# Kernel tuning notes

Measured on AMD Instinct MI355X. Metric: run time of the kernel, lower is better.

The kernel has to match this reference:

```python
import jax, jax.numpy as jnp
import numpy as np

EPS = 1e-8

def l2norm(x, axis):
    # matches torch: x / (sqrt(sum(x^2)) + eps)
    return x / (jnp.sqrt(jnp.sum(x * x, axis=axis, keepdims=True)) + EPS)

def setup_inputs() -> dict:
    key = jax.random.key(0)
    kq, kc, kwq, kbq, kwk, kbk = jax.random.split(key, 6)
    B, QL, SL, D = 128, 512, 1024, 1024
    query = jax.random.normal(kq, (B, QL, D), dtype=jnp.float32)
    context = jax.random.normal(kc, (B, SL, D), dtype=jnp.float32)
    s = 1.0 / np.sqrt(D)
    Wq = jax.random.uniform(kwq, (D, D), jnp.float32, -s, s)
    bq = jax.random.uniform(kbq, (D,), jnp.float32, -s, s)
    Wk = jax.random.uniform(kwk, (D, D), jnp.float32, -s, s)
    bk = jax.random.uniform(kbk, (D,), jnp.float32, -s, s)
    return {"query": query, "context": context, "Wq": Wq, "bq": bq,
            "Wk": Wk, "bk": bk, "smooth": 9.0}

def reference(query, context, Wq, bq, Wk, bk, smooth):
    # linear projections (nn.Linear: x @ W^T + b)
    sim_k = jnp.einsum('bsd,ed->bse', context, Wk) + bk   # (B, SL, D)
    sim_q = jnp.einsum('bqd,ed->bqe', query, Wq) + bq     # (B, QL, D)
    # scores: bmm(sim_k, sim_q^T) -> (B, SL, QL)
    attn = jnp.einsum('bse,bqe->bsq', sim_k, sim_q)
    attn = jnp.where(attn >= 0, attn, 0.1 * attn)          # LeakyReLU(0.1)
    attn = l2norm(attn, axis=2)                            # over queryL dim
    # transpose -> (B, QL, SL), scale, softmax over sourceL
    attn = jax.nn.softmax(attn.transpose(0, 2, 1) * smooth, axis=2)
    # weighted sum of raw context (sim_v = context; fcv unused in original)
    wc = jnp.einsum('bqs,bsd->bqd', attn, context)         # (B, QL, D)
    return l2norm(wc, axis=-1)
```

## Files before the change

kernel.cpp:

```cpp
#include <hip/hip_runtime.h>
#include <hip/hip_bf16.h>

typedef __attribute__((ext_vector_type(8))) short bf16x8;
typedef __attribute__((ext_vector_type(4))) float f32x4;
typedef __attribute__((ext_vector_type(4))) unsigned short u16x4;
typedef __attribute__((ext_vector_type(8))) unsigned short u16x8;

#define DEVINL static __device__ __forceinline__

DEVINL unsigned short f2bf(float f) {
  union { float f; unsigned u; } a; a.f = f;
  return (unsigned short)((a.u + 0x7fffu + ((a.u >> 16) & 1u)) >> 16);
}
DEVINL float bf2f(unsigned short s) {
  union { unsigned u; float f; } a; a.u = ((unsigned)s) << 16; return a.f;
}

typedef __attribute__((address_space(1))) const unsigned char ga_u8;
typedef __attribute__((address_space(3))) unsigned char ls_u8;

constexpr int KD = 1024;
constexpr int NKT = KD / 64;


#define STAGE(b_, mat_, kt_) do { \
    const unsigned short* src_ = (mat_) == 0 ? Az : Bz; \
    const int br_ = (mat_) == 0 ? m0 : n0; \
    char* dst_ = lds + (b_) * 65536 + (mat_) * 32768; \
    _Pragma("unroll") \
    for (int i_ = 0; i_ < 4; ++i_) { \
      const unsigned short* g_ = src_ + (size_t)(br_ + i_ * 64 + sr) * KD + (kt_) * 64 + gc * 8; \
      __builtin_amdgcn_global_load_lds((ga_u8*)g_, (ls_u8*)(dst_ + (i_ * 512 + wv * 64) * 16), 16, 0, 0); \
    } \
  } while (0)

#define STAGE2(b_, kt_) do { STAGE(b_, 0, kt_); STAGE(b_, 1, kt_); } while (0)

#define KSUB(b_, ks_, STG) do { \
    const char* pA_ = lds + (b_) * 65536; \
    const char* pB_ = pA_ + 32768; \
    const int co_ = (((ks_) * 4 + kg) ^ (ml & 7)) << 4; \
    bf16x8 af_[8], bf_[4]; \
    _Pragma("unroll") \
    for (int mi = 0; mi < 8; ++mi) \
      af_[mi] = *(const bf16x8*)(pA_ + (wm * 128 + mi * 16 + ml) * 128 + co_); \
    _Pragma("unroll") \
    for (int ni = 0; ni < 4; ++ni) \
      bf_[ni] = *(const bf16x8*)(pB_ + (wn * 64 + ni * 16 + ml) * 128 + co_); \
    STG; \
    __builtin_amdgcn_s_setprio(1); \
    _Pragma("unroll") \
    for (int mi = 0; mi < 8; ++mi) \
    _Pragma("unroll") \
    for (int ni = 0; ni < 4; ++ni) \
      acc[mi][ni] = __builtin_amdgcn_mfma_f32_16x16x32_bf16(af_[mi], bf_[ni], acc[mi][ni], 0, 0, 0); \
    __builtin_amdgcn_s_setprio(0); \
  } while (0)

template<int MODE>
__global__ __launch_bounds__(512, 2) void gemm8(
    const unsigned short* __restrict__ A, const unsigned short* __restrict__ B,
    const float* __restrict__ bias, void* __restrict__ Cv,
    float* __restrict__ rnorm2, int mtiles,
    long long sAz, long long sBz, long long sCz, long long sRz, long long sBiasz)
{
  alignas(16) __shared__ char lds[131072];

  const int tid = threadIdx.x;
  const int lane = tid & 63;
  const int wv = tid >> 6;
  const int wm = wv >> 2;
  const int wn = wv & 3;
  const int kg = lane >> 4;
  const int ml = lane & 15;

  const int nwg = (int)gridDim.x;
  const int bid = (int)blockIdx.x;
  const int w = (bid & 7) * (nwg >> 3) + (bid >> 3);
  const int bpz = mtiles * 4;
  const int z = w / bpz;
  const int rem = w - z * bpz;
  const int mt = rem >> 2, nt = rem & 3;
  const int m0 = mt * 256, n0 = nt * 256;

  const unsigned short* Az = A + (size_t)z * (size_t)sAz;
  const unsigned short* Bz = B + (size_t)z * (size_t)sBz;

  const int sr = tid >> 3;
  const int gc = (tid & 7) ^ (sr & 7);

  f32x4 acc[8][4];
  const f32x4 zero4 = {0.f, 0.f, 0.f, 0.f};
#pragma unroll
  for (int i = 0; i < 8; ++i)
#pragma unroll
    for (int j = 0; j < 4; ++j) acc[i][j] = zero4;

  STAGE2(0, 0);
  asm volatile("s_waitcnt vmcnt(0)" ::: "memory");
  __builtin_amdgcn_s_barrier();

  for (int t = 0; t < NKT; ++t) {
    const int cur = t & 1;
    const int nxt = cur ^ 1;
    if (t + 1 < NKT) {
      KSUB(cur, 0, STAGE2(nxt, t + 1));
      KSUB(cur, 1, );
    } else {
      KSUB(cur, 0, );
      KSUB(cur, 1, );
    }
    asm volatile("s_waitcnt vmcnt(0)" ::: "memory");
    __builtin_amdgcn_s_barrier();
  }

  float* ew = (float*)(lds + wv * 4352);
  const int erow = lane >> 3;
  const int ec8 = (lane & 7) * 8;
  const int ncol0 = n0 + wn * 64;

  if (MODE == 1 || MODE == 5) {
    const float* cb = bias + (size_t)z * (size_t)sBiasz;
    f32x4 cb4[8];
#pragma unroll
    for (int mi = 0; mi < 8; ++mi)
      cb4[mi] = *(const f32x4*)(cb + m0 + wm * 128 + mi * 16 + kg * 4);
    float* rn = rnorm2 + (size_t)z * (size_t)sRz;
#pragma unroll
    for (int ni = 0; ni < 4; ++ni) {
      float cs = 0.f;
#pragma unroll
      for (int mi = 0; mi < 8; ++mi)
#pragma unroll
        for (int j = 0; j < 4; ++j) {
          float v = acc[mi][ni][j] + cb4[mi][j];
          v = v >= 0.f ? v : 0.1f * v;
          acc[mi][ni][j] = v;
          cs += v * v;
        }
      cs += __shfl_xor(cs, 16);
      cs += __shfl_xor(cs, 32);
      if (kg == 0) atomicAdd(&rn[ncol0 + ni * 16 + ml], cs);
    }
  }

  f32x4 bv0 = zero4, bv1 = zero4;
  if (MODE == 0) {
    bv0 = *(const f32x4*)(bias + ncol0 + ec8);
    bv1 = *(const f32x4*)(bias + ncol0 + ec8 + 4);
  }

  float* rsq = (MODE == 4) ? rnorm2 + (size_t)z * (size_t)sRz : nullptr;

#pragma unroll
  for (int mi = 0; mi < 8; ++mi) {
#pragma unroll
    for (int ni = 0; ni < 4; ++ni)
#pragma unroll
      for (int j = 0; j < 4; ++j)
        ew[(kg * 4 + j) * 68 + ni * 16 + ml] = acc[mi][ni][j];
    const int rb = m0 + wm * 128 + mi * 16;
#pragma unroll
    for (int i = 0; i < 2; ++i) {
      const int r = erow + 8 * i;
      f32x4 x = *(const f32x4*)(&ew[r * 68 + ec8]);
      f32x4 y = *(const f32x4*)(&ew[r * 68 + ec8 + 4]);
      if (MODE == 4) {
        float ss = x[0]*x[0] + x[1]*x[1] + x[2]*x[2] + x[3]*x[3] +
                   y[0]*y[0] + y[1]*y[1] + y[2]*y[2] + y[3]*y[3];
        ss += __shfl_xor(ss, 1);
        ss += __shfl_xor(ss, 2);
        ss += __shfl_xor(ss, 4);
        if ((lane & 7) == 0) atomicAdd(&rsq[rb + r], ss);
      }
      if (MODE == 0 || MODE == 3 || MODE == 4 || MODE == 5) {
        unsigned short* C = (unsigned short*)Cv + (size_t)z * (size_t)sCz;
        union { unsigned short s[8]; u16x8 v; } u;
        u.s[0]=f2bf(x[0]+bv0[0]); u.s[1]=f2bf(x[1]+bv0[1]);
        u.s[2]=f2bf(x[2]+bv0[2]); u.s[3]=f2bf(x[3]+bv0[3]);
        u.s[4]=f2bf(y[0]+bv1[0]); u.s[5]=f2bf(y[1]+bv1[1]);
        u.s[6]=f2bf(y[2]+bv1[2]); u.s[7]=f2bf(y[3]+bv1[3]);
        *(u16x8*)(C + (size_t)(rb + r) * 1024 + ncol0 + ec8) = u.v;
      } else {
        float* C = (float*)Cv + (size_t)z * (size_t)sCz;
        *(f32x4*)(C + (size_t)(rb + r) * 1024 + ncol0 + ec8) = x;
        *(f32x4*)(C + (size_t)(rb + r) * 1024 + ncol0 + ec8 + 4) = y;
      }
    }
  }
}

__global__ __launch_bounds__(256) void wT_k(
    const float* __restrict__ W, unsigned short* __restrict__ WT)
{
  __shared__ float tile[32][36];
  const int t = threadIdx.x;
  const int e0 = blockIdx.x * 32, d0 = blockIdx.y * 32;
  const int r = t >> 3, c4 = (t & 7) * 4;
  f32x4 v = *(const f32x4*)(W + (size_t)(e0 + r) * 1024 + d0 + c4);
  *(f32x4*)(&tile[r][c4]) = v;
  __syncthreads();
  u16x4 o;
  o[0] = f2bf(tile[c4 + 0][r]); o[1] = f2bf(tile[c4 + 1][r]);
  o[2] = f2bf(tile[c4 + 2][r]); o[3] = f2bf(tile[c4 + 3][r]);
  *(u16x4*)(WT + (size_t)(d0 + r) * 1024 + e0 + c4) = o;
}

__global__ __launch_bounds__(256) void convert_ctx_k(
    const float* __restrict__ src, unsigned short* __restrict__ dstT,
    unsigned short* __restrict__ dstR)
{
  __shared__ float tile[32][36];
  const int t = threadIdx.x;
  const int s0 = blockIdx.x * 32, d0 = blockIdx.y * 32;
  const float* S = src + (size_t)blockIdx.z * 1048576;
  unsigned short* DT = dstT + (size_t)blockIdx.z * 1048576;
  unsigned short* DR = dstR + (size_t)blockIdx.z * 1048576;
  const int s = t >> 3, d4 = (t & 7) * 4;
  f32x4 v = *(const f32x4*)(S + (size_t)(s0 + s) * 1024 + d0 + d4);
  u16x4 r;
  r[0] = f2bf(v[0]); r[1] = f2bf(v[1]); r[2] = f2bf(v[2]); r[3] = f2bf(v[3]);
  *(u16x4*)(DR + (size_t)(s0 + s) * 1024 + d0 + d4) = r;
  *(f32x4*)(&tile[s][d4]) = v;
  __syncthreads();
  const int d = t >> 3, s4 = (t & 7) * 4;
  u16x4 o;
  o[0] = f2bf(tile[s4 + 0][d]); o[1] = f2bf(tile[s4 + 1][d]);
  o[2] = f2bf(tile[s4 + 2][d]); o[3] = f2bf(tile[s4 + 3][d]);
  *(u16x4*)(DT + (size_t)(d0 + d) * 1024 + s0 + s4) = o;
}

__global__ __launch_bounds__(256) void rowdot_k(
    const unsigned short* __restrict__ Mbf, const float* __restrict__ vec,
    float* __restrict__ outv)
{
  __shared__ float shs[4];
  const int t = threadIdx.x;
  const unsigned short* row = Mbf + (size_t)blockIdx.x * 1024;
  u16x4 a = *(const u16x4*)(row + t * 4);
  f32x4 b = *(const f32x4*)(vec + t * 4);
  float d = bf2f(a[0]) * b[0] + bf2f(a[1]) * b[1] +
            bf2f(a[2]) * b[2] + bf2f(a[3]) * b[3];
#pragma unroll
  for (int o = 32; o; o >>= 1) d += __shfl_xor(d, o);
  if ((t & 63) == 0) shs[t >> 6] = d;
  __syncthreads();
  if (t == 0) outv[blockIdx.x] = shs[0] + shs[1] + shs[2] + shs[3];
}

__global__ __launch_bounds__(256) void dot1_k(
    const float* __restrict__ a, const float* __restrict__ b,
    float* __restrict__ outv)
{
  __shared__ float shs[4];
  const int t = threadIdx.x;
  f32x4 x = ((const f32x4*)a)[t];
  f32x4 y = ((const f32x4*)b)[t];
  float d = x[0]*y[0] + x[1]*y[1] + x[2]*y[2] + x[3]*y[3];
#pragma unroll
  for (int o = 32; o; o >>= 1) d += __shfl_xor(d, o);
  if ((t & 63) == 0) shs[t >> 6] = d;
  __syncthreads();
  if (t == 0) outv[0] = shs[0] + shs[1] + shs[2] + shs[3];
}

__global__ __launch_bounds__(128) void cvtq_dot_k(
    const float* __restrict__ q, const float* __restrict__ vb,
    const float* __restrict__ bqbk, unsigned short* __restrict__ qbf,
    float* __restrict__ cq)
{
  __shared__ float sh[2];
  const int t = threadIdx.x;
  const size_t base = (size_t)blockIdx.x * 1024 + t * 8;
  f32x4 x = *(const f32x4*)(q + base);
  f32x4 y = *(const f32x4*)(q + base + 4);
  f32x4 v0 = *(const f32x4*)(vb + t * 8);
  f32x4 v1 = *(const f32x4*)(vb + t * 8 + 4);
  union { unsigned short s[8]; u16x8 v; } u;
  u.s[0]=f2bf(x[0]); u.s[1]=f2bf(x[1]); u.s[2]=f2bf(x[2]); u.s[3]=f2bf(x[3]);
  u.s[4]=f2bf(y[0]); u.s[5]=f2bf(y[1]); u.s[6]=f2bf(y[2]); u.s[7]=f2bf(y[3]);
  *(u16x8*)(qbf + base) = u.v;
  float d = x[0]*v0[0] + x[1]*v0[1] + x[2]*v0[2] + x[3]*v0[3] +
            y[0]*v1[0] + y[1]*v1[1] + y[2]*v1[2] + y[3]*v1[3];
#pragma unroll
  for (int o = 32; o; o >>= 1) d += __shfl_xor(d, o);
  if ((t & 63) == 0) sh[t >> 6] = d;
  __syncthreads();
  if (t == 0) cq[blockIdx.x] = sh[0] + sh[1] + bqbk[0];
}

__global__ __launch_bounds__(256) void softmax_k(
    const unsigned short* __restrict__ S, const float* __restrict__ rnorm2,
    const float* __restrict__ smoothp, unsigned short* __restrict__ P)
{
  __shared__ float shm[4], shs[4];
  const int t = threadIdx.x;
  const int z = blockIdx.x >> 9;
  const float sm = *smoothp;
  u16x4 sr = ((const u16x4*)(S + (size_t)blockIdx.x * 1024))[t];
  f32x4 r4 = ((const f32x4*)(rnorm2 + (size_t)z * 1024))[t];
  f32x4 lg;
  lg[0] = sm * bf2f(sr[0]) / (sqrtf(r4[0]) + 1e-8f);
  lg[1] = sm * bf2f(sr[1]) / (sqrtf(r4[1]) + 1e-8f);
  lg[2] = sm * bf2f(sr[2]) / (sqrtf(r4[2]) + 1e-8f);
  lg[3] = sm * bf2f(sr[3]) / (sqrtf(r4[3]) + 1e-8f);
  float mx = fmaxf(fmaxf(lg[0], lg[1]), fmaxf(lg[2], lg[3]));
#pragma unroll
  for (int o = 32; o; o >>= 1) mx = fmaxf(mx, __shfl_xor(mx, o));
  if ((t & 63) == 0) shm[t >> 6] = mx;
  __syncthreads();
  mx = fmaxf(fmaxf(shm[0], shm[1]), fmaxf(shm[2], shm[3]));
  f32x4 e;
  e[0] = __expf(lg[0] - mx); e[1] = __expf(lg[1] - mx);
  e[2] = __expf(lg[2] - mx); e[3] = __expf(lg[3] - mx);
  float sum = e[0] + e[1] + e[2] + e[3];
#pragma unroll
  for (int o = 32; o; o >>= 1) sum += __shfl_xor(sum, o);
  if ((t & 63) == 0) shs[t >> 6] = sum;
  __syncthreads();
  sum = shs[0] + shs[1] + shs[2] + shs[3];
  float inv = 1.f / sum;
  u16x4 p;
  p[0] = f2bf(e[0] * inv); p[1] = f2bf(e[1] * inv);
  p[2] = f2bf(e[2] * inv); p[3] = f2bf(e[3] * inv);
  ((u16x4*)(P + (size_t)blockIdx.x * 1024))[t] = p;
}

__global__ __launch_bounds__(256) void l2fin_k(
    const unsigned short* __restrict__ Wb, const float* __restrict__ rssq,
    float* __restrict__ O)
{
  const int t = threadIdx.x;
  const size_t base = (size_t)blockIdx.x * 1024 + t * 4;
  u16x4 w = *(const u16x4*)(Wb + base);
  float inv = 1.f / (sqrtf(rssq[blockIdx.x]) + 1e-8f);
  f32x4 o = { bf2f(w[0]) * inv, bf2f(w[1]) * inv,
              bf2f(w[2]) * inv, bf2f(w[3]) * inv };
  *(f32x4*)(O + base) = o;
}

extern "C" void kernel_launch(void* const* d_in, const int* in_sizes, int n_in,
                              void* d_out, int out_size, void* d_ws, size_t ws_size,
                              hipStream_t stream)
{
  (void)in_sizes; (void)n_in; (void)out_size;
  const float* query   = (const float*)d_in[0];
  const float* context = (const float*)d_in[1];
  const float* Wq = (const float*)d_in[2];
  const float* bq = (const float*)d_in[3];
  const float* Wk = (const float*)d_in[4];
  const float* bk = (const float*)d_in[5];
  const float* smooth = (const float*)d_in[6];
  float* out = (float*)d_out;

  const int B = 128, QL = 512, SL = 1024, D = 1024;

  const size_t perB =
      (size_t)QL * D * 2 + (size_t)SL * D * 2 + (size_t)D * SL * 2 +
      (size_t)QL * D * 2 + (size_t)QL * SL * 2 +
      (size_t)SL * 4 + (size_t)QL * 4 + (size_t)QL * 4 + 4096;
  const size_t fixed = 3 * (size_t)D * D * 2 + 2 * (size_t)D * 4 + 16384;
  size_t usable = ws_size > fixed ? ws_size - fixed : 0;
  int C = (int)(usable / perB);
  if (C > B) C = B;
  if (C < 1) C = 1;

  char* p = (char*)d_ws;
  auto alloc = [&](size_t bytes) {
    char* r = p; p += (bytes + 255) & ~(size_t)255; return r;
  };
  unsigned short* wqT  = (unsigned short*)alloc((size_t)D * D * 2);
  unsigned short* wkT  = (unsigned short*)alloc((size_t)D * D * 2);
  unsigned short* WuT  = (unsigned short*)alloc((size_t)D * D * 2);
  float* cu   = (float*)alloc((size_t)D * 4);
  float* vb   = (float*)alloc((size_t)D * 4);
  float* bqbk = (float*)alloc(256);
  unsigned short* qbf  = (unsigned short*)alloc((size_t)C * QL * D * 2);
  unsigned short* ctxbf= (unsigned short*)alloc((size_t)C * SL * D * 2);
  unsigned short* ctxT = (unsigned short*)alloc((size_t)C * D * SL * 2);
  unsigned short* ubf  = (unsigned short*)alloc((size_t)C * QL * D * 2);
  unsigned short* Sbuf = (unsigned short*)alloc((size_t)C * QL * SL * 2);
  float* rn   = (float*)alloc((size_t)C * SL * 4);
  float* cq   = (float*)alloc((size_t)C * QL * 4);
  float* rsq  = (float*)alloc((size_t)C * QL * 4);

  wT_k<<<dim3(32, 32), 256, 0, stream>>>(Wq, wqT);
  wT_k<<<dim3(32, 32), 256, 0, stream>>>(Wk, wkT);
  rowdot_k<<<dim3(D), 256, 0, stream>>>(wkT, bq, cu);
  rowdot_k<<<dim3(D), 256, 0, stream>>>(wqT, bk, vb);
  dot1_k<<<dim3(1), 256, 0, stream>>>(bq, bk, bqbk);
  gemm8<3><<<dim3(16), 512, 0, stream>>>(
      wkT, wqT, nullptr, WuT, nullptr, 4, 0, 0, 0, 0, 0);

  for (int b0 = 0; b0 < B; b0 += C) {
    const int Cc = (B - b0) < C ? (B - b0) : C;
    hipMemsetAsync(rn, 0, (size_t)Cc * SL * 4, stream);
    hipMemsetAsync(rsq, 0, (size_t)Cc * QL * 4, stream);
    cvtq_dot_k<<<dim3(Cc * QL), 128, 0, stream>>>(
        query + (size_t)b0 * QL * D, vb, bqbk, qbf, cq);
    convert_ctx_k<<<dim3(32, 32, Cc), 256, 0, stream>>>(
        context + (size_t)b0 * SL * D, ctxT, ctxbf);
    gemm8<0><<<dim3(Cc * 8), 512, 0, stream>>>(
        qbf, WuT, cu, ubf, nullptr, 2,
        (long long)QL * D, 0, (long long)QL * D, 0, 0);
    gemm8<5><<<dim3(Cc * 8), 512, 0, stream>>>(
        ubf, ctxbf, cq, Sbuf, rn, 2,
        (long long)QL * D, (long long)SL * D, (long long)QL * SL,
        (long long)SL, (long long)QL);
    softmax_k<<<Cc * QL, 256, 0, stream>>>(Sbuf, rn, smooth, ubf );
    gemm8<4><<<dim3(Cc * 8), 512, 0, stream>>>(
        ubf , ctxT, nullptr, Sbuf , rsq, 2,
        (long long)QL * SL, (long long)D * SL, (long long)QL * D,
        (long long)QL, 0);
    l2fin_k<<<dim3(Cc * QL), 256, 0, stream>>>(
        Sbuf, rsq, out + (size_t)b0 * QL * D);
  }
}
```

Baseline: 962.4 us.

## Triple-buffer A tiles with staggered A/B prefetch in GEMM main loop

Replaces the double-buffered K loop with a software pipeline that uses three LDS slots for A and two for B. A is prefetched two tiles ahead and B one tile ahead, and the loop waits only until outstanding loads drop to four instead of draining to zero. The goal is to hide global-to-LDS latency behind MFMA work. It also removes dead epilogue branches and merges the two memsets into one by placing the buffers next to each other. LDS per block grows to 160KB, which may limit occupancy below the requested two blocks per CU.

New measurement: 995.4 us. +3.4%, slower.

```diff
diff --git a/kernel.cpp b/kernel.cpp
--- a/kernel.cpp
+++ b/kernel.cpp
@@ -20,25 +20,33 @@
 typedef __attribute__((address_space(3))) unsigned char ls_u8;
 
 constexpr int KD = 1024;
-constexpr int NKT = KD / 64;
-
-
-#define STAGE(b_, mat_, kt_) do { \
-    const unsigned short* src_ = (mat_) == 0 ? Az : Bz; \
-    const int br_ = (mat_) == 0 ? m0 : n0; \
-    char* dst_ = lds + (b_) * 65536 + (mat_) * 32768; \
+
+
+#define VM4 asm volatile("s_waitcnt vmcnt(4)" ::: "memory")
+#define VM0 asm volatile("s_waitcnt vmcnt(0)" ::: "memory")
+#define BARR __builtin_amdgcn_s_barrier()
+
+#define STAGE_A(slot_, kt_) do { \
+    char* dst_ = lds + (slot_) * 32768; \
     _Pragma("unroll") \
     for (int i_ = 0; i_ < 4; ++i_) { \
-      const unsigned short* g_ = src_ + (size_t)(br_ + i_ * 64 + sr) * KD + (kt_) * 64 + gc * 8; \
+      const unsigned short* g_ = Az + (size_t)(m0 + i_ * 64 + sr) * KD + (kt_) * 64 + gc * 8; \
       __builtin_amdgcn_global_load_lds((ga_u8*)g_, (ls_u8*)(dst_ + (i_ * 512 + wv * 64) * 16), 16, 0, 0); \
     } \
   } while (0)
 
-#define STAGE2(b_, kt_) do { STAGE(b_, 0, kt_); STAGE(b_, 1, kt_); } while (0)
-
-#define KSUB(b_, ks_, STG) do { \
-    const char* pA_ = lds + (b_) * 65536; \
-    const char* pB_ = pA_ + 32768; \
+#define STAGE_B(slot_, kt_) do { \
+    char* dst_ = lds + 98304 + (slot_) * 32768; \
+    _Pragma("unroll") \
+    for (int i_ = 0; i_ < 4; ++i_) { \
+      const unsigned short* g_ = Bz + (size_t)(n0 + i_ * 64 + sr) * KD + (kt_) * 64 + gc * 8; \
+      __builtin_amdgcn_global_load_lds((ga_u8*)g_, (ls_u8*)(dst_ + (i_ * 512 + wv * 64) * 16), 16, 0, 0); \
+    } \
+  } while (0)
+
+#define KSUB(as_, bs_, ks_, STG) do { \
+    const char* pA_ = lds + (as_) * 32768; \
+    const char* pB_ = lds + 98304 + (bs_) * 32768; \
     const int co_ = (((ks_) * 4 + kg) ^ (ml & 7)) << 4; \
     bf16x8 af_[8], bf_[4]; \
     _Pragma("unroll") \
@@ -55,6 +63,12 @@
     for (int ni = 0; ni < 4; ++ni) \
       acc[mi][ni] = __builtin_amdgcn_mfma_f32_16x16x32_bf16(af_[mi], bf_[ni], acc[mi][ni], 0, 0, 0); \
     __builtin_amdgcn_s_setprio(0); \
+  } while (0)
+
+#define TILE_STD(as_, bs_, bs1_, as2_, t_) do { \
+    KSUB(as_, bs_, 0, STAGE_B(bs1_, (t_) + 1)); \
+    KSUB(as_, bs_, 1, STAGE_A(as2_, (t_) + 2)); \
+    VM4; BARR; \
   } while (0)
 
 template<int MODE>
@@ -64,7 +78,7 @@
     float* __restrict__ rnorm2, int mtiles,
     long long sAz, long long sBz, long long sCz, long long sRz, long long sBiasz)
 {
-  alignas(16) __shared__ char lds[131072];
+  alignas(16) __shared__ char lds[163840];
 
   const int tid = threadIdx.x;
   const int lane = tid & 63;
@@ -96,30 +110,32 @@
 #pragma unroll
     for (int j = 0; j < 4; ++j) acc[i][j] = zero4;
 
-  STAGE2(0, 0);
-  asm volatile("s_waitcnt vmcnt(0)" ::: "memory");
-  __builtin_amdgcn_s_barrier();
-
-  for (int t = 0; t < NKT; ++t) {
-    const int cur = t & 1;
-    const int nxt = cur ^ 1;
-    if (t + 1 < NKT) {
-      KSUB(cur, 0, STAGE2(nxt, t + 1));
-      KSUB(cur, 1, );
-    } else {
-      KSUB(cur, 0, );
-      KSUB(cur, 1, );
-    }
-    asm volatile("s_waitcnt vmcnt(0)" ::: "memory");
-    __builtin_amdgcn_s_barrier();
+  STAGE_A(0, 0); STAGE_B(0, 0); STAGE_A(1, 1);
+  VM4; BARR;
+
+  for (int t6 = 0; t6 < 12; t6 += 6) {
+    TILE_STD(0, 0, 1, 2, t6 + 0);
+    TILE_STD(1, 1, 0, 0, t6 + 1);
+    TILE_STD(2, 0, 1, 1, t6 + 2);
+    TILE_STD(0, 1, 0, 2, t6 + 3);
+    TILE_STD(1, 0, 1, 0, t6 + 4);
+    TILE_STD(2, 1, 0, 1, t6 + 5);
   }
+  TILE_STD(0, 0, 1, 2, 12);
+  TILE_STD(1, 1, 0, 0, 13);
+  KSUB(2, 0, 0, STAGE_B(1, 15));
+  KSUB(2, 0, 1, );
+  VM0; BARR;
+  KSUB(0, 1, 0, );
+  KSUB(0, 1, 1, );
+  BARR;
 
   float* ew = (float*)(lds + wv * 4352);
   const int erow = lane >> 3;
   const int ec8 = (lane & 7) * 8;
   const int ncol0 = n0 + wn * 64;
 
-  if (MODE == 1 || MODE == 5) {
+  if (MODE == 5) {
     const float* cb = bias + (size_t)z * (size_t)sBiasz;
     f32x4 cb4[8];
 #pragma unroll
@@ -173,19 +189,13 @@
         ss += __shfl_xor(ss, 4);
         if ((lane & 7) == 0) atomicAdd(&rsq[rb + r], ss);
       }
-      if (MODE == 0 || MODE == 3 || MODE == 4 || MODE == 5) {
-        unsigned short* C = (unsigned short*)Cv + (size_t)z * (size_t)sCz;
-        union { unsigned short s[8]; u16x8 v; } u;
-        u.s[0]=f2bf(x[0]+bv0[0]); u.s[1]=f2bf(x[1]+bv0[1]);
-        u.s[2]=f2bf(x[2]+bv0[2]); u.s[3]=f2bf(x[3]+bv0[3]);
-        u.s[4]=f2bf(y[0]+bv1[0]); u.s[5]=f2bf(y[1]+bv1[1]);
-        u.s[6]=f2bf(y[2]+bv1[2]); u.s[7]=f2bf(y[3]+bv1[3]);
-        *(u16x8*)(C + (size_t)(rb + r) * 1024 + ncol0 + ec8) = u.v;
-      } else {
-        float* C = (float*)Cv + (size_t)z * (size_t)sCz;
-        *(f32x4*)(C + (size_t)(rb + r) * 1024 + ncol0 + ec8) = x;
-        *(f32x4*)(C + (size_t)(rb + r) * 1024 + ncol0 + ec8 + 4) = y;
-      }
+      unsigned short* C = (unsigned short*)Cv + (size_t)z * (size_t)sCz;
+      union { unsigned short s[8]; u16x8 v; } u;
+      u.s[0]=f2bf(x[0]+bv0[0]); u.s[1]=f2bf(x[1]+bv0[1]);
+      u.s[2]=f2bf(x[2]+bv0[2]); u.s[3]=f2bf(x[3]+bv0[3]);
+      u.s[4]=f2bf(y[0]+bv1[0]); u.s[5]=f2bf(y[1]+bv1[1]);
+      u.s[6]=f2bf(y[2]+bv1[2]); u.s[7]=f2bf(y[3]+bv1[3]);
+      *(u16x8*)(C + (size_t)(rb + r) * 1024 + ncol0 + ec8) = u.v;
     }
   }
 }
@@ -381,8 +391,9 @@
   unsigned short* ubf  = (unsigned short*)alloc((size_t)C * QL * D * 2);
   unsigned short* Sbuf = (unsigned short*)alloc((size_t)C * QL * SL * 2);
   float* rn   = (float*)alloc((size_t)C * SL * 4);
+  float* rsq  = (float*)alloc((size_t)C * QL * 4);
   float* cq   = (float*)alloc((size_t)C * QL * 4);
-  float* rsq  = (float*)alloc((size_t)C * QL * 4);
+  const size_t zspan = (size_t)((char*)(rsq + (size_t)C * QL) - (char*)rn);
 
   wT_k<<<dim3(32, 32), 256, 0, stream>>>(Wq, wqT);
   wT_k<<<dim3(32, 32), 256, 0, stream>>>(Wk, wkT);
@@ -394,8 +405,7 @@
 
   for (int b0 = 0; b0 < B; b0 += C) {
     const int Cc = (B - b0) < C ? (B - b0) : C;
-    hipMemsetAsync(rn, 0, (size_t)Cc * SL * 4, stream);
-    hipMemsetAsync(rsq, 0, (size_t)Cc * QL * 4, stream);
+    hipMemsetAsync(rn, 0, zspan, stream);
     cvtq_dot_k<<<dim3(Cc * QL), 128, 0, stream>>>(
         query + (size_t)b0 * QL * D, vb, bqbk, qbf, cq);
     convert_ctx_k<<<dim3(32, 32, Cc), 256, 0, stream>>>(
```
